# Kernel tuning notes

Measured on AMD Instinct MI355X. Metric: run time of the kernel, lower is better.

Reference implementation:

```python
import jax, jax.numpy as jnp
import numpy as np

N = 8192        # n_nodes
F = 256         # n_features
RES_H = 512     # n_res_hidden
REP_H = 256     # n_rep_hidden
EMB = 128       # embed_dim
E = 262144      # n_edges
GAMMA = 0.1


def setup_inputs() -> dict:
    key = jax.random.key(0)
    ks = jax.random.split(key, 20)
    w = lambda k, shape, s=0.05: (jax.random.normal(k, shape, jnp.float32) * s)
    return {
        "x": jax.random.normal(ks[0], (N, F), jnp.float32),
        "edge_index": jax.random.randint(ks[1], (2, E), 0, N),
        # res_model: Linear(N,RES_H)+ReLU, Linear(RES_H,F)+ReLU
        "res_W1": w(ks[2], (N, RES_H)), "res_b1": jnp.zeros((RES_H,), jnp.float32),
        "res_W2": w(ks[3], (RES_H, F)), "res_b2": jnp.zeros((F,), jnp.float32),
        "fc_W1": w(ks[4], (F, REP_H)), "fc_b1": jnp.zeros((REP_H,), jnp.float32),
        "fc_W2": w(ks[5], (REP_H, REP_H)), "fc_b2": jnp.zeros((REP_H,), jnp.float32),
        # rep_gcn: GCNConv(F,REP_H,norm=False), GCNConv(REP_H,REP_H), GCNConv(REP_H,EMB)
        "g_W0": w(ks[6], (F, REP_H)), "g_b0": jnp.zeros((REP_H,), jnp.float32),
        "g_W1": w(ks[7], (REP_H, REP_H)), "g_b1": jnp.zeros((REP_H,), jnp.float32),
        "g_W2": w(ks[8], (REP_H, EMB)), "g_b2": jnp.zeros((EMB,), jnp.float32),
        # dec_fc: Linear(EMB,REP_H)+ReLU, Linear(REP_H,F)+ReLU
        "dec_W1": w(ks[9], (EMB, REP_H)), "dec_b1": jnp.zeros((REP_H,), jnp.float32),
        "dec_W2": w(ks[10], (REP_H, F)), "dec_b2": jnp.zeros((F,), jnp.float32),
    }


def _gcn(h, src, dst, W, b, normalize):
    """PyG GCNConv: transform then aggregate src->dst; sym-norm with self loops if normalize."""
    h = h @ W
    if normalize:
        ones = jnp.ones(src.shape[0], h.dtype)
        deg = jax.ops.segment_sum(ones, dst, num_segments=N) + 1.0  # +1 self loop
        dinv = jax.lax.rsqrt(deg)
        coef = dinv[src] * dinv[dst]
        agg = jax.ops.segment_sum(h[src] * coef[:, None], dst, num_segments=N)
        agg = agg + h * (dinv * dinv)[:, None]  # self-loop message
    else:
        agg = jax.ops.segment_sum(h[src], dst, num_segments=N)
    return agg + b


def _fwd(x, edge_index, res_W1, res_b1, res_W2, res_b2, fc_W1, fc_b1, fc_W2, fc_b2,
         g_W0, g_b0, g_W1, g_b1, g_W2, g_b2, dec_W1, dec_b1, dec_W2, dec_b2):
    relu = jax.nn.relu
    src, dst = edge_index[0], edge_index[1]
    # dense adjacency (to_dense_adj accumulates edge weights = 1)
    A = jnp.zeros((N, N), x.dtype).at[src, dst].add(1.0)
    # residual model over adjacency rows
    R = relu(relu(A @ res_W1 + res_b1) @ res_W2 + res_b2)  # [N, F]
    # GCN layer 0 (normalize=False)
    H = relu(_gcn(x, src, dst, g_W0, g_b0, False))
    # layer 1
    R_l = relu(R @ fc_W1 + fc_b1)
    H = relu(_gcn(H * jnp.exp(-GAMMA * R_l), src, dst, g_W1, g_b1, True))
    # layer 2
    R_l = relu(R_l @ fc_W2 + fc_b2)
    H = relu(_gcn(H * jnp.exp(-GAMMA * R_l), src, dst, g_W2, g_b2, True))  # [N, EMB]
    X_hat = relu(relu(H @ dec_W1 + dec_b1) @ dec_W2 + dec_b2)  # [N, F]
    A_hat = H @ H.T  # [N, N]
    return X_hat, A_hat, R


def reference(x, edge_index, res_W1, res_b1, res_W2, res_b2, fc_W1, fc_b1, fc_W2, fc_b2,
              g_W0, g_b0, g_W1, g_b1, g_W2, g_b2, dec_W1, dec_b1, dec_W2, dec_b2):
    return _fwd(x, edge_index, res_W1, res_b1, res_W2, res_b2, fc_W1, fc_b1, fc_W2, fc_b2,
                g_W0, g_b0, g_W1, g_b1, g_W2, g_b2, dec_W1, dec_b1, dec_W2, dec_b2)
```

## Files before the change

kernel.cpp:

```cpp
#include <hip/hip_runtime.h>
#include <cstddef>
#include <cstdint>
#include <math.h>

#define NN   8192
#define FF   256
#define RESH 512
#define REPH 256
#define EMBD 128
#define EE   262144
#define GAMMA_ 0.1f

typedef __attribute__((ext_vector_type(8))) short bf16x8;
typedef __attribute__((ext_vector_type(4))) float f32x4;
typedef __attribute__((ext_vector_type(4))) short s16x4;

__device__ inline void f2hilo(float x, short& h, short& l) {
  unsigned u = __float_as_uint(x);
  unsigned r = u + 0x7FFFu + ((u >> 16) & 1u);
  h = (short)(r >> 16);
  float hf = __uint_as_float(r & 0xFFFF0000u);
  float lf = x - hf;
  unsigned u2 = __float_as_uint(lf);
  unsigned r2 = u2 + 0x7FFFu + ((u2 >> 16) & 1u);
  l = (short)(r2 >> 16);
}


__global__ void count_kernel(const int* __restrict__ ei, int* __restrict__ cnt_src,
                             int* __restrict__ cnt_dst) {
  int e = blockIdx.x * blockDim.x + threadIdx.x;
  if (e < EE) {
    atomicAdd(&cnt_src[ei[e]], 1);
    atomicAdd(&cnt_dst[ei[EE + e]], 1);
  }
}

__global__ void scan_kernel(const int* __restrict__ cnt_src, const int* __restrict__ cnt_dst,
                            int* __restrict__ off_src, int* __restrict__ off_dst) {
  const int* cnt = blockIdx.x ? cnt_dst : cnt_src;
  int* off = blockIdx.x ? off_dst : off_src;
  __shared__ int sm[1024];
  int carry = 0;
  for (int ch = 0; ch < NN / 1024; ++ch) {
    int idx = ch * 1024 + threadIdx.x;
    int v = cnt[idx];
    int x = v;
    sm[threadIdx.x] = x;
    __syncthreads();
    for (int ofs = 1; ofs < 1024; ofs <<= 1) {
      int y = (threadIdx.x >= ofs) ? sm[threadIdx.x - ofs] : 0;
      __syncthreads();
      x += y;
      sm[threadIdx.x] = x;
      __syncthreads();
    }
    off[idx] = x - v + carry;
    carry += sm[1023];
    __syncthreads();
  }
  if (threadIdx.x == 0) off[NN] = carry;
}

__global__ void fill_kernel(const int* __restrict__ ei, const int* __restrict__ off_src,
                            const int* __restrict__ off_dst, int* __restrict__ cur_src,
                            int* __restrict__ cur_dst, int* __restrict__ adj_src,
                            int* __restrict__ adj_dst) {
  int e = blockIdx.x * blockDim.x + threadIdx.x;
  if (e < EE) {
    int s = ei[e], d = ei[EE + e];
    int ps = atomicAdd(&cur_src[s], 1);
    adj_src[off_src[s] + ps] = d;
    int pd = atomicAdd(&cur_dst[d], 1);
    adj_dst[off_dst[d] + pd] = s;
  }
}

__global__ void dinv_kernel(const int* __restrict__ cnt_dst, float* __restrict__ dinv) {
  int n = blockIdx.x * blockDim.x + threadIdx.x;
  if (n < NN) dinv[n] = rsqrtf((float)cnt_dst[n] + 1.0f);
}

__global__ __launch_bounds__(256) void s1_kernel(const float* __restrict__ W1,
    const float* __restrict__ b1, const int* __restrict__ off_src,
    const int* __restrict__ adj_src, short* __restrict__ S1h, short* __restrict__ S1l) {
  int i = blockIdx.x, t = threadIdx.x;
  int beg = off_src[i], end = off_src[i + 1];
  float a0 = 0.f, a1 = 0.f;
#pragma unroll 4
  for (int k = beg; k < end; ++k) {
    int d = adj_src[k];
    const float* row = W1 + (size_t)d * RESH;
    a0 += row[t];
    a1 += row[t + 256];
  }
  float v0 = fmaxf(a0 + b1[t], 0.f);
  float v1 = fmaxf(a1 + b1[t + 256], 0.f);
  short hh, ll;
  f2hilo(v0, hh, ll);
  S1h[(size_t)i * RESH + t] = hh;
  S1l[(size_t)i * RESH + t] = ll;
  f2hilo(v1, hh, ll);
  S1h[(size_t)i * RESH + t + 256] = hh;
  S1l[(size_t)i * RESH + t + 256] = ll;
}

__global__ __launch_bounds__(256) void agg0_fused(const float* __restrict__ h,
    const float* __restrict__ b, const float* __restrict__ mod,
    const int* __restrict__ off_dst, const int* __restrict__ adj_dst,
    short* __restrict__ oh, short* __restrict__ ol) {
  int d = blockIdx.x, t = threadIdx.x;
  int beg = off_dst[d], end = off_dst[d + 1];
  float acc = 0.f;
#pragma unroll 4
  for (int k = beg; k < end; ++k) {
    int s = adj_dst[k];
    acc += h[(size_t)s * REPH + t];
  }
  size_t o = (size_t)d * REPH + t;
  float v = fmaxf(acc + b[t], 0.f) * expf(-GAMMA_ * mod[o]);
  short hh, ll;
  f2hilo(v, hh, ll);
  oh[o] = hh;
  ol[o] = ll;
}

__global__ void aggn_fused(const float* __restrict__ h, const float* __restrict__ b,
    const float* __restrict__ dinv, const float* __restrict__ mod,
    const int* __restrict__ off_dst, const int* __restrict__ adj_dst,
    short* __restrict__ oh, short* __restrict__ ol, int C) {
  int d = blockIdx.x, t = threadIdx.x;
  int beg = off_dst[d], end = off_dst[d + 1];
  float acc = 0.f;
#pragma unroll 4
  for (int k = beg; k < end; ++k) {
    int s = adj_dst[k];
    acc += h[(size_t)s * C + t] * dinv[s];
  }
  float dd = dinv[d];
  size_t o = (size_t)d * C + t;
  float v = fmaxf(acc * dd + h[o] * dd * dd + b[t], 0.f);
  if (mod) v *= expf(-GAMMA_ * mod[o]);
  short hh, ll;
  f2hilo(v, hh, ll);
  oh[o] = hh;
  ol[o] = ll;
}

struct WDesc { const float* src; short* h; short* l; int K; int N; };
struct WTab { WDesc d[8]; };

__global__ void prep_w(WTab tab) {
  WDesc d = tab.d[blockIdx.y];
  int total = d.K * d.N;
  for (int i = blockIdx.x * 256 + threadIdx.x; i < total; i += 128 * 256) {
    int n = i / d.K, k = i - n * d.K;
    float x = d.src[(size_t)k * d.N + n];
    short hh, ll;
    f2hilo(x, hh, ll);
    d.h[i] = hh;
    d.l[i] = ll;
  }
}

__global__ void conv_split(const float* __restrict__ in, short* __restrict__ oh,
                           short* __restrict__ ol) {
  int i = (blockIdx.x * 256 + threadIdx.x) * 4;
  f32x4 v = *(const f32x4*)(in + i);
  s16x4 vh, vl;
#pragma unroll
  for (int j = 0; j < 4; ++j) {
    short hh, ll;
    f2hilo(v[j], hh, ll);
    vh[j] = hh;
    vl[j] = ll;
  }
  *(s16x4*)(oh + i) = vh;
  *(s16x4*)(ol + i) = vl;
}

template<int CB>
__global__ __launch_bounds__(256) void gemmS(const short* __restrict__ Ah,
    const short* __restrict__ Al, const short* __restrict__ Wh,
    const short* __restrict__ Wl, const float* __restrict__ bias, int doRelu,
    float* __restrict__ outF, short* __restrict__ outH, short* __restrict__ outL,
    int K, int Nc) {
  const int w = threadIdx.x >> 6, l = threadIdx.x & 63;
  const int lr = l & 15, lk = l >> 4;
  const int m0 = blockIdx.y * 64 + w * 16;
  const int n0 = blockIdx.x * (CB * 16);
  f32x4 acc[CB] = {};
  const int nks = K >> 5;
  for (int ks = 0; ks < nks; ++ks) {
    const int k0 = (ks << 5) + (lk << 3);
    size_t aoff = (size_t)(m0 + lr) * K + k0;
    bf16x8 ah = *(const bf16x8*)(Ah + aoff);
    bf16x8 al = *(const bf16x8*)(Al + aoff);
#pragma unroll
    for (int cb = 0; cb < CB; ++cb) {
      size_t boff = (size_t)(n0 + (cb << 4) + lr) * K + k0;
      bf16x8 bh = *(const bf16x8*)(Wh + boff);
      bf16x8 bl = *(const bf16x8*)(Wl + boff);
      acc[cb] = __builtin_amdgcn_mfma_f32_16x16x32_bf16(ah, bh, acc[cb], 0, 0, 0);
      acc[cb] = __builtin_amdgcn_mfma_f32_16x16x32_bf16(al, bh, acc[cb], 0, 0, 0);
      acc[cb] = __builtin_amdgcn_mfma_f32_16x16x32_bf16(ah, bl, acc[cb], 0, 0, 0);
    }
  }
#pragma unroll
  for (int cb = 0; cb < CB; ++cb) {
    int col = n0 + (cb << 4) + lr;
    float bv = bias ? bias[col] : 0.f;
#pragma unroll
    for (int r = 0; r < 4; ++r) {
      int row = m0 + (lk << 2) + r;
      float v = acc[cb][r] + bv;
      if (doRelu) v = fmaxf(v, 0.f);
      size_t off = (size_t)row * Nc + col;
      if (outF) outF[off] = v;
      if (outH) {
        short hh, ll;
        f2hilo(v, hh, ll);
        outH[off] = hh;
        outL[off] = ll;
      }
    }
  }
}

__global__ __launch_bounds__(256) void ahat_sym(const short* __restrict__ Hh,
    const short* __restrict__ Hl, float* __restrict__ C) {
  __shared__ float sm[128][129];
  int z = blockIdx.x;
  int b = (int)((sqrtf(8.f * (float)z + 1.f) - 1.f) * 0.5f);
  while ((b + 1) * (b + 2) / 2 <= z) ++b;
  while (b * (b + 1) / 2 > z) --b;
  int a = z - b * (b + 1) / 2;
  const int bi = a * 128, bj = b * 128;
  const bool mirror = (a != b);
  const int w = threadIdx.x >> 6, l = threadIdx.x & 63;
  const int lr = l & 15, lk = l >> 4;
  const int ri = w * 32;
  f32x4 acc[2][8] = {};
#pragma unroll
  for (int ks = 0; ks < 4; ++ks) {
    const int k0 = (ks << 5) + (lk << 3);
    bf16x8 ah[2], al[2];
#pragma unroll
    for (int rb = 0; rb < 2; ++rb) {
      size_t off = (size_t)(bi + ri + (rb << 4) + lr) * EMBD + k0;
      ah[rb] = *(const bf16x8*)(Hh + off);
      al[rb] = *(const bf16x8*)(Hl + off);
    }
#pragma unroll
    for (int cb = 0; cb < 8; ++cb) {
      size_t off = (size_t)(bj + (cb << 4) + lr) * EMBD + k0;
      bf16x8 bh = *(const bf16x8*)(Hh + off);
      bf16x8 bl = *(const bf16x8*)(Hl + off);
#pragma unroll
      for (int rb = 0; rb < 2; ++rb) {
        acc[rb][cb] = __builtin_amdgcn_mfma_f32_16x16x32_bf16(ah[rb], bh, acc[rb][cb], 0, 0, 0);
        acc[rb][cb] = __builtin_amdgcn_mfma_f32_16x16x32_bf16(al[rb], bh, acc[rb][cb], 0, 0, 0);
        acc[rb][cb] = __builtin_amdgcn_mfma_f32_16x16x32_bf16(ah[rb], bl, acc[rb][cb], 0, 0, 0);
      }
    }
  }
#pragma unroll
  for (int rb = 0; rb < 2; ++rb)
#pragma unroll
    for (int cb = 0; cb < 8; ++cb) {
      int r0 = ri + (rb << 4) + (lk << 2);
      int c0 = (cb << 4) + lr;
#pragma unroll
      for (int r = 0; r < 4; ++r) {
        float v = acc[rb][cb][r];
        C[(size_t)(bi + r0 + r) * NN + bj + c0] = v;
        if (mirror) sm[r0 + r][c0] = v;
      }
    }
  if (mirror) {
    __syncthreads();
    for (int idx = threadIdx.x; idx < 128 * 128; idx += 256) {
      int jr = idx >> 7, c = idx & 127;
      C[(size_t)(bj + jr) * NN + bi + c] = sm[c][jr];
    }
  }
}


extern "C" void kernel_launch(void* const* d_in, const int* in_sizes, int n_in,
                              void* d_out, int out_size, void* d_ws, size_t ws_size,
                              hipStream_t stream) {
  const float* x      = (const float*)d_in[0];
  const int*   ei     = (const int*)d_in[1];
  const float* res_W1 = (const float*)d_in[2];
  const float* res_b1 = (const float*)d_in[3];
  const float* res_W2 = (const float*)d_in[4];
  const float* res_b2 = (const float*)d_in[5];
  const float* fc_W1  = (const float*)d_in[6];
  const float* fc_b1  = (const float*)d_in[7];
  const float* fc_W2  = (const float*)d_in[8];
  const float* fc_b2  = (const float*)d_in[9];
  const float* g_W0   = (const float*)d_in[10];
  const float* g_b0   = (const float*)d_in[11];
  const float* g_W1   = (const float*)d_in[12];
  const float* g_b1   = (const float*)d_in[13];
  const float* g_W2   = (const float*)d_in[14];
  const float* g_b2   = (const float*)d_in[15];
  const float* dec_W1 = (const float*)d_in[16];
  const float* dec_b1 = (const float*)d_in[17];
  const float* dec_W2 = (const float*)d_in[18];
  const float* dec_b2 = (const float*)d_in[19];

  float* out   = (float*)d_out;
  float* X_hat = out;
  float* A_hat = out + (size_t)NN * FF;
  float* R     = A_hat + (size_t)NN * NN;

  char* ws = (char*)d_ws;
  size_t o = 0;
  auto alloc = [&](size_t bytes) -> void* {
    void* p = ws + o;
    o += (bytes + 1023) & ~(size_t)1023;
    return p;
  };
  int* cnt_src = (int*)alloc(NN * 4);
  int* cnt_dst = (int*)alloc(NN * 4);
  int* cur_src = (int*)alloc(NN * 4);
  int* cur_dst = (int*)alloc(NN * 4);
  int* off_src = (int*)alloc((NN + 1) * 4);
  int* off_dst = (int*)alloc((NN + 1) * 4);
  int* adj_src = (int*)alloc((size_t)EE * 4);
  int* adj_dst = (int*)alloc((size_t)EE * 4);
  float* dinv  = (float*)alloc(NN * 4);
  short* Wt_h  = (short*)alloc(524288 * 2);
  short* Wt_l  = (short*)alloc(524288 * 2);
  const size_t SLAB = (size_t)8 * 1024 * 1024;
  char* slabA = (char*)alloc(SLAB);
  char* slabB = (char*)alloc(SLAB);
  char* slabC = (char*)alloc(SLAB);
  char* slabD = (char*)alloc(SLAB);
  short* S1h = (short*)slabA;
  short* Xh  = (short*)slabA;            short* Xl  = (short*)(slabA + SLAB / 2);
  short* M1h = (short*)slabA;            short* M1l = (short*)(slabA + SLAB / 2);
  short* M2h = (short*)slabA;            short* M2l = (short*)(slabA + SLAB / 2);
  short* D1h = (short*)slabA;            short* D1l = (short*)(slabA + SLAB / 2);
  short* S1l = (short*)slabB;
  float* B3f = (float*)slabB;
  float* B4f = (float*)slabB;
  float* G2f = (float*)slabB;
  short* Rh  = (short*)slabC;            short* Rl  = (short*)(slabC + SLAB / 2);
  float* B1f = (float*)slabC;
  float* G1f = (float*)slabC;
  short* B3h = (short*)slabD;            short* B3l = (short*)(slabD + SLAB / 2);
  short* Hh  = (short*)slabD;            short* Hl  = (short*)(slabD + (size_t)2 * 1024 * 1024);

  const int o_resW2 = 0;
  const int o_fcW1  = 131072;
  const int o_fcW2  = 196608;
  const int o_gW0   = 262144;
  const int o_gW1   = 327680;
  const int o_gW2   = 393216;
  const int o_decW1 = 425984;
  const int o_decW2 = 458752;

  hipMemsetAsync(cnt_src, 0, (size_t)NN * 4 * 4, stream);

  count_kernel<<<EE / 256, 256, 0, stream>>>(ei, cnt_src, cnt_dst);
  scan_kernel<<<2, 1024, 0, stream>>>(cnt_src, cnt_dst, off_src, off_dst);
  fill_kernel<<<EE / 256, 256, 0, stream>>>(ei, off_src, off_dst, cur_src, cur_dst,
                                            adj_src, adj_dst);
  dinv_kernel<<<NN / 256, 256, 0, stream>>>(cnt_dst, dinv);

  WTab tab;
  tab.d[0] = {res_W2, Wt_h + o_resW2, Wt_l + o_resW2, RESH, FF};
  tab.d[1] = {fc_W1,  Wt_h + o_fcW1,  Wt_l + o_fcW1,  FF,   REPH};
  tab.d[2] = {fc_W2,  Wt_h + o_fcW2,  Wt_l + o_fcW2,  REPH, REPH};
  tab.d[3] = {g_W0,   Wt_h + o_gW0,   Wt_l + o_gW0,   FF,   REPH};
  tab.d[4] = {g_W1,   Wt_h + o_gW1,   Wt_l + o_gW1,   REPH, REPH};
  tab.d[5] = {g_W2,   Wt_h + o_gW2,   Wt_l + o_gW2,   REPH, EMBD};
  tab.d[6] = {dec_W1, Wt_h + o_decW1, Wt_l + o_decW1, EMBD, REPH};
  tab.d[7] = {dec_W2, Wt_h + o_decW2, Wt_l + o_decW2, REPH, FF};
  prep_w<<<dim3(128, 8), 256, 0, stream>>>(tab);

  s1_kernel<<<NN, 256, 0, stream>>>(res_W1, res_b1, off_src, adj_src, S1h, S1l);
  gemmS<8><<<dim3(2, 128), 256, 0, stream>>>(S1h, S1l, Wt_h + o_resW2, Wt_l + o_resW2,
      res_b2, 1, R, Rh, Rl, RESH, FF);
  gemmS<8><<<dim3(2, 128), 256, 0, stream>>>(Rh, Rl, Wt_h + o_fcW1, Wt_l + o_fcW1,
      fc_b1, 1, B3f, B3h, B3l, FF, REPH);
  conv_split<<<(NN * FF) / 1024, 256, 0, stream>>>(x, Xh, Xl);
  gemmS<8><<<dim3(2, 128), 256, 0, stream>>>(Xh, Xl, Wt_h + o_gW0, Wt_l + o_gW0,
      nullptr, 0, B1f, nullptr, nullptr, FF, REPH);
  agg0_fused<<<NN, REPH, 0, stream>>>(B1f, g_b0, B3f, off_dst, adj_dst, M1h, M1l);
  gemmS<8><<<dim3(2, 128), 256, 0, stream>>>(M1h, M1l, Wt_h + o_gW1, Wt_l + o_gW1,
      nullptr, 0, G1f, nullptr, nullptr, REPH, REPH);
  gemmS<8><<<dim3(2, 128), 256, 0, stream>>>(B3h, B3l, Wt_h + o_fcW2, Wt_l + o_fcW2,
      fc_b2, 1, B4f, nullptr, nullptr, REPH, REPH);
  aggn_fused<<<NN, REPH, 0, stream>>>(G1f, g_b1, dinv, B4f, off_dst, adj_dst,
                                      M2h, M2l, REPH);
  gemmS<4><<<dim3(2, 128), 256, 0, stream>>>(M2h, M2l, Wt_h + o_gW2, Wt_l + o_gW2,
      nullptr, 0, G2f, nullptr, nullptr, REPH, EMBD);
  aggn_fused<<<NN, EMBD, 0, stream>>>(G2f, g_b2, dinv, nullptr, off_dst, adj_dst,
                                      Hh, Hl, EMBD);
  gemmS<8><<<dim3(2, 128), 256, 0, stream>>>(Hh, Hl, Wt_h + o_decW1, Wt_l + o_decW1,
      dec_b1, 1, nullptr, D1h, D1l, EMBD, REPH);
  gemmS<8><<<dim3(2, 128), 256, 0, stream>>>(D1h, D1l, Wt_h + o_decW2, Wt_l + o_decW2,
      dec_b2, 1, X_hat, nullptr, nullptr, REPH, FF);
  ahat_sym<<<2080, 256, 0, stream>>>(Hh, Hl, A_hat);
}
```

Before: 800.2 us.

## Vectorize gather-aggregation kernels and split edge lists across wavefronts

The four gather kernels (adjacency-row sum and three GCN aggregations) are rewritten so each lane loads float4 or float2 chunks of a neighbour row. The edge list is split across the block's wavefronts, each unrolled by four, and partial sums are reduced through shared memory. The aim is more memory-level parallelism and fewer load instructions per edge. dinv is now computed inside the scan kernel, which removes one launch. The cost is a shared-memory reduction plus a sync, and only one wavefront does the epilogue.

```diff
diff --git a/kernel.cpp b/kernel.cpp
--- a/kernel.cpp
+++ b/kernel.cpp
@@ -13,7 +13,9 @@
 
 typedef __attribute__((ext_vector_type(8))) short bf16x8;
 typedef __attribute__((ext_vector_type(4))) float f32x4;
+typedef __attribute__((ext_vector_type(2))) float f32x2;
 typedef __attribute__((ext_vector_type(4))) short s16x4;
+typedef __attribute__((ext_vector_type(2))) short s16x2;
 
 __device__ inline void f2hilo(float x, short& h, short& l) {
   unsigned u = __float_as_uint(x);
@@ -37,7 +39,8 @@
 }
 
 __global__ void scan_kernel(const int* __restrict__ cnt_src, const int* __restrict__ cnt_dst,
-                            int* __restrict__ off_src, int* __restrict__ off_dst) {
+                            int* __restrict__ off_src, int* __restrict__ off_dst,
+                            float* __restrict__ dinv) {
   const int* cnt = blockIdx.x ? cnt_dst : cnt_src;
   int* off = blockIdx.x ? off_dst : off_src;
   __shared__ int sm[1024];
@@ -45,6 +48,7 @@
   for (int ch = 0; ch < NN / 1024; ++ch) {
     int idx = ch * 1024 + threadIdx.x;
     int v = cnt[idx];
+    if (blockIdx.x) dinv[idx] = rsqrtf((float)v + 1.0f);
     int x = v;
     sm[threadIdx.x] = x;
     __syncthreads();
@@ -76,75 +80,181 @@
   }
 }
 
-__global__ void dinv_kernel(const int* __restrict__ cnt_dst, float* __restrict__ dinv) {
-  int n = blockIdx.x * blockDim.x + threadIdx.x;
-  if (n < NN) dinv[n] = rsqrtf((float)cnt_dst[n] + 1.0f);
-}
-
-__global__ __launch_bounds__(256) void s1_kernel(const float* __restrict__ W1,
+__global__ __launch_bounds__(256) void s1_v2(const float* __restrict__ W1,
     const float* __restrict__ b1, const int* __restrict__ off_src,
     const int* __restrict__ adj_src, short* __restrict__ S1h, short* __restrict__ S1l) {
-  int i = blockIdx.x, t = threadIdx.x;
-  int beg = off_src[i], end = off_src[i + 1];
-  float a0 = 0.f, a1 = 0.f;
-#pragma unroll 4
-  for (int k = beg; k < end; ++k) {
-    int d = adj_src[k];
-    const float* row = W1 + (size_t)d * RESH;
-    a0 += row[t];
-    a1 += row[t + 256];
-  }
-  float v0 = fmaxf(a0 + b1[t], 0.f);
-  float v1 = fmaxf(a1 + b1[t + 256], 0.f);
-  short hh, ll;
-  f2hilo(v0, hh, ll);
-  S1h[(size_t)i * RESH + t] = hh;
-  S1l[(size_t)i * RESH + t] = ll;
-  f2hilo(v1, hh, ll);
-  S1h[(size_t)i * RESH + t + 256] = hh;
-  S1l[(size_t)i * RESH + t + 256] = ll;
-}
-
-__global__ __launch_bounds__(256) void agg0_fused(const float* __restrict__ h,
+  __shared__ f32x4 p2[2][64];
+  const int i = blockIdx.x, w = threadIdx.x >> 6, lane = threadIdx.x & 63;
+  const int half = w & 1, par = w >> 1;
+  const int col = half * 256 + lane * 4;
+  const float* base = W1 + col;
+  const int beg = off_src[i], end = off_src[i + 1];
+  f32x4 acc = {};
+  int k = beg + par;
+  for (; k + 6 < end; k += 8) {
+    int s0 = adj_src[k], s1 = adj_src[k + 2], s2 = adj_src[k + 4], s3 = adj_src[k + 6];
+    f32x4 h0 = *(const f32x4*)(base + (size_t)s0 * RESH);
+    f32x4 h1 = *(const f32x4*)(base + (size_t)s1 * RESH);
+    f32x4 h2 = *(const f32x4*)(base + (size_t)s2 * RESH);
+    f32x4 h3 = *(const f32x4*)(base + (size_t)s3 * RESH);
+    acc += h0 + h1 + h2 + h3;
+  }
+  for (; k < end; k += 2) {
+    int s = adj_src[k];
+    acc += *(const f32x4*)(base + (size_t)s * RESH);
+  }
+  if (par == 1) p2[half][lane] = acc;
+  __syncthreads();
+  if (par == 0) {
+    acc += p2[half][lane];
+    f32x4 bb = *(const f32x4*)(b1 + col);
+    s16x4 vh, vl;
+#pragma unroll
+    for (int j = 0; j < 4; ++j) {
+      float v = fmaxf(acc[j] + bb[j], 0.f);
+      short hh, ll;
+      f2hilo(v, hh, ll);
+      vh[j] = hh; vl[j] = ll;
+    }
+    size_t o = (size_t)i * RESH + col;
+    *(s16x4*)(S1h + o) = vh;
+    *(s16x4*)(S1l + o) = vl;
+  }
+}
+
+__global__ __launch_bounds__(256) void agg0_v2(const float* __restrict__ h,
     const float* __restrict__ b, const float* __restrict__ mod,
     const int* __restrict__ off_dst, const int* __restrict__ adj_dst,
     short* __restrict__ oh, short* __restrict__ ol) {
-  int d = blockIdx.x, t = threadIdx.x;
-  int beg = off_dst[d], end = off_dst[d + 1];
-  float acc = 0.f;
-#pragma unroll 4
-  for (int k = beg; k < end; ++k) {
+  __shared__ f32x4 part[3][64];
+  const int d = blockIdx.x, w = threadIdx.x >> 6, lane = threadIdx.x & 63;
+  const float* base = h + lane * 4;
+  const int beg = off_dst[d], end = off_dst[d + 1];
+  f32x4 acc = {};
+  int k = beg + w;
+  for (; k + 12 < end; k += 16) {
+    int s0 = adj_dst[k], s1 = adj_dst[k + 4], s2 = adj_dst[k + 8], s3 = adj_dst[k + 12];
+    f32x4 h0 = *(const f32x4*)(base + (size_t)s0 * REPH);
+    f32x4 h1 = *(const f32x4*)(base + (size_t)s1 * REPH);
+    f32x4 h2 = *(const f32x4*)(base + (size_t)s2 * REPH);
+    f32x4 h3 = *(const f32x4*)(base + (size_t)s3 * REPH);
+    acc += h0 + h1 + h2 + h3;
+  }
+  for (; k < end; k += 4) {
     int s = adj_dst[k];
-    acc += h[(size_t)s * REPH + t];
-  }
-  size_t o = (size_t)d * REPH + t;
-  float v = fmaxf(acc + b[t], 0.f) * expf(-GAMMA_ * mod[o]);
-  short hh, ll;
-  f2hilo(v, hh, ll);
-  oh[o] = hh;
-  ol[o] = ll;
-}
-
-__global__ void aggn_fused(const float* __restrict__ h, const float* __restrict__ b,
-    const float* __restrict__ dinv, const float* __restrict__ mod,
+    acc += *(const f32x4*)(base + (size_t)s * REPH);
+  }
+  if (w) part[w - 1][lane] = acc;
+  __syncthreads();
+  if (w == 0) {
+    acc += part[0][lane] + part[1][lane] + part[2][lane];
+    size_t o = (size_t)d * REPH + lane * 4;
+    f32x4 bb = *(const f32x4*)(b + lane * 4);
+    f32x4 mm = *(const f32x4*)(mod + o);
+    s16x4 vh, vl;
+#pragma unroll
+    for (int j = 0; j < 4; ++j) {
+      float v = fmaxf(acc[j] + bb[j], 0.f) * expf(-GAMMA_ * mm[j]);
+      short hh, ll;
+      f2hilo(v, hh, ll);
+      vh[j] = hh; vl[j] = ll;
+    }
+    *(s16x4*)(oh + o) = vh;
+    *(s16x4*)(ol + o) = vl;
+  }
+}
+
+__global__ __launch_bounds__(256) void aggn256_v2(const float* __restrict__ h,
+    const float* __restrict__ b, const float* __restrict__ dinv,
+    const float* __restrict__ mod, const int* __restrict__ off_dst,
+    const int* __restrict__ adj_dst, short* __restrict__ oh, short* __restrict__ ol) {
+  __shared__ f32x4 part[3][64];
+  const int d = blockIdx.x, w = threadIdx.x >> 6, lane = threadIdx.x & 63;
+  const float* base = h + lane * 4;
+  const int beg = off_dst[d], end = off_dst[d + 1];
+  f32x4 acc = {};
+  int k = beg + w;
+  for (; k + 12 < end; k += 16) {
+    int s0 = adj_dst[k], s1 = adj_dst[k + 4], s2 = adj_dst[k + 8], s3 = adj_dst[k + 12];
+    float d0 = dinv[s0], d1 = dinv[s1], d2 = dinv[s2], d3 = dinv[s3];
+    f32x4 h0 = *(const f32x4*)(base + (size_t)s0 * REPH);
+    f32x4 h1 = *(const f32x4*)(base + (size_t)s1 * REPH);
+    f32x4 h2 = *(const f32x4*)(base + (size_t)s2 * REPH);
+    f32x4 h3 = *(const f32x4*)(base + (size_t)s3 * REPH);
+    acc += h0 * d0 + h1 * d1 + h2 * d2 + h3 * d3;
+  }
+  for (; k < end; k += 4) {
+    int s = adj_dst[k];
+    acc += *(const f32x4*)(base + (size_t)s * REPH) * dinv[s];
+  }
+  if (w) part[w - 1][lane] = acc;
+  __syncthreads();
+  if (w == 0) {
+    acc += part[0][lane] + part[1][lane] + part[2][lane];
+    const float dd = dinv[d];
+    size_t o = (size_t)d * REPH + lane * 4;
+    f32x4 bb = *(const f32x4*)(b + lane * 4);
+    f32x4 self = *(const f32x4*)(h + o);
+    s16x4 vh, vl;
+    if (mod) {
+      f32x4 mm = *(const f32x4*)(mod + o);
+#pragma unroll
+      for (int j = 0; j < 4; ++j) {
+        float v = fmaxf(acc[j] * dd + self[j] * dd * dd + bb[j], 0.f) * expf(-GAMMA_ * mm[j]);
+        short hh, ll; f2hilo(v, hh, ll); vh[j] = hh; vl[j] = ll;
+      }
+    } else {
+#pragma unroll
+      for (int j = 0; j < 4; ++j) {
+        float v = fmaxf(acc[j] * dd + self[j] * dd * dd + bb[j], 0.f);
+        short hh, ll; f2hilo(v, hh, ll); vh[j] = hh; vl[j] = ll;
+      }
+    }
+    *(s16x4*)(oh + o) = vh;
+    *(s16x4*)(ol + o) = vl;
+  }
+}
+
+__global__ __launch_bounds__(256) void aggn128_v2(const float* __restrict__ h,
+    const float* __restrict__ b, const float* __restrict__ dinv,
     const int* __restrict__ off_dst, const int* __restrict__ adj_dst,
-    short* __restrict__ oh, short* __restrict__ ol, int C) {
-  int d = blockIdx.x, t = threadIdx.x;
-  int beg = off_dst[d], end = off_dst[d + 1];
-  float acc = 0.f;
-#pragma unroll 4
-  for (int k = beg; k < end; ++k) {
+    short* __restrict__ oh, short* __restrict__ ol) {
+  __shared__ f32x2 part[3][64];
+  const int d = blockIdx.x, w = threadIdx.x >> 6, lane = threadIdx.x & 63;
+  const float* base = h + lane * 2;
+  const int beg = off_dst[d], end = off_dst[d + 1];
+  f32x2 acc = {};
+  int k = beg + w;
+  for (; k + 12 < end; k += 16) {
+    int s0 = adj_dst[k], s1 = adj_dst[k + 4], s2 = adj_dst[k + 8], s3 = adj_dst[k + 12];
+    float d0 = dinv[s0], d1 = dinv[s1], d2 = dinv[s2], d3 = dinv[s3];
+    f32x2 h0 = *(const f32x2*)(base + (size_t)s0 * EMBD);
+    f32x2 h1 = *(const f32x2*)(base + (size_t)s1 * EMBD);
+    f32x2 h2 = *(const f32x2*)(base + (size_t)s2 * EMBD);
+    f32x2 h3 = *(const f32x2*)(base + (size_t)s3 * EMBD);
+    acc += h0 * d0 + h1 * d1 + h2 * d2 + h3 * d3;
+  }
+  for (; k < end; k += 4) {
     int s = adj_dst[k];
-    acc += h[(size_t)s * C + t] * dinv[s];
-  }
-  float dd = dinv[d];
-  size_t o = (size_t)d * C + t;
-  float v = fmaxf(acc * dd + h[o] * dd * dd + b[t], 0.f);
-  if (mod) v *= expf(-GAMMA_ * mod[o]);
-  short hh, ll;
-  f2hilo(v, hh, ll);
-  oh[o] = hh;
-  ol[o] = ll;
+    acc += *(const f32x2*)(base + (size_t)s * EMBD) * dinv[s];
+  }
+  if (w) part[w - 1][lane] = acc;
+  __syncthreads();
+  if (w == 0) {
+    acc += part[0][lane] + part[1][lane] + part[2][lane];
+    const float dd = dinv[d];
+    size_t o = (size_t)d * EMBD + lane * 2;
+    f32x2 bb = *(const f32x2*)(b + lane * 2);
+    f32x2 self = *(const f32x2*)(h + o);
+    s16x2 vh, vl;
+#pragma unroll
+    for (int j = 0; j < 2; ++j) {
+      float v = fmaxf(acc[j] * dd + self[j] * dd * dd + bb[j], 0.f);
+      short hh, ll; f2hilo(v, hh, ll); vh[j] = hh; vl[j] = ll;
+    }
+    *(s16x2*)(oh + o) = vh;
+    *(s16x2*)(ol + o) = vl;
+  }
 }
 
 struct WDesc { const float* src; short* h; short* l; int K; int N; };
@@ -366,10 +476,9 @@
   hipMemsetAsync(cnt_src, 0, (size_t)NN * 4 * 4, stream);
 
   count_kernel<<<EE / 256, 256, 0, stream>>>(ei, cnt_src, cnt_dst);
-  scan_kernel<<<2, 1024, 0, stream>>>(cnt_src, cnt_dst, off_src, off_dst);
+  scan_kernel<<<2, 1024, 0, stream>>>(cnt_src, cnt_dst, off_src, off_dst, dinv);
   fill_kernel<<<EE / 256, 256, 0, stream>>>(ei, off_src, off_dst, cur_src, cur_dst,
                                             adj_src, adj_dst);
-  dinv_kernel<<<NN / 256, 256, 0, stream>>>(cnt_dst, dinv);
 
   WTab tab;
   tab.d[0] = {res_W2, Wt_h + o_resW2, Wt_l + o_resW2, RESH, FF};
@@ -382,7 +491,7 @@
   tab.d[7] = {dec_W2, Wt_h + o_decW2, Wt_l + o_decW2, REPH, FF};
   prep_w<<<dim3(128, 8), 256, 0, stream>>>(tab);
 
-  s1_kernel<<<NN, 256, 0, stream>>>(res_W1, res_b1, off_src, adj_src, S1h, S1l);
+  s1_v2<<<NN, 256, 0, stream>>>(res_W1, res_b1, off_src, adj_src, S1h, S1l);
   gemmS<8><<<dim3(2, 128), 256, 0, stream>>>(S1h, S1l, Wt_h + o_resW2, Wt_l + o_resW2,
       res_b2, 1, R, Rh, Rl, RESH, FF);
   gemmS<8><<<dim3(2, 128), 256, 0, stream>>>(Rh, Rl, Wt_h + o_fcW1, Wt_l + o_fcW1,
@@ -390,17 +499,15 @@
   conv_split<<<(NN * FF) / 1024, 256, 0, stream>>>(x, Xh, Xl);
   gemmS<8><<<dim3(2, 128), 256, 0, stream>>>(Xh, Xl, Wt_h + o_gW0, Wt_l + o_gW0,
       nullptr, 0, B1f, nullptr, nullptr, FF, REPH);
-  agg0_fused<<<NN, REPH, 0, stream>>>(B1f, g_b0, B3f, off_dst, adj_dst, M1h, M1l);
+  agg0_v2<<<NN, 256, 0, stream>>>(B1f, g_b0, B3f, off_dst, adj_dst, M1h, M1l);
   gemmS<8><<<dim3(2, 128), 256, 0, stream>>>(M1h, M1l, Wt_h + o_gW1, Wt_l + o_gW1,
       nullptr, 0, G1f, nullptr, nullptr, REPH, REPH);
   gemmS<8><<<dim3(2, 128), 256, 0, stream>>>(B3h, B3l, Wt_h + o_fcW2, Wt_l + o_fcW2,
       fc_b2, 1, B4f, nullptr, nullptr, REPH, REPH);
-  aggn_fused<<<NN, REPH, 0, stream>>>(G1f, g_b1, dinv, B4f, off_dst, adj_dst,
-                                      M2h, M2l, REPH);
+  aggn256_v2<<<NN, 256, 0, stream>>>(G1f, g_b1, dinv, B4f, off_dst, adj_dst, M2h, M2l);
   gemmS<4><<<dim3(2, 128), 256, 0, stream>>>(M2h, M2l, Wt_h + o_gW2, Wt_l + o_gW2,
       nullptr, 0, G2f, nullptr, nullptr, REPH, EMBD);
-  aggn_fused<<<NN, EMBD, 0, stream>>>(G2f, g_b2, dinv, nullptr, off_dst, adj_dst,
-                                      Hh, Hl, EMBD);
+  aggn128_v2<<<NN, 256, 0, stream>>>(G2f, g_b2, dinv, off_dst, adj_dst, Hh, Hl);
   gemmS<8><<<dim3(2, 128), 256, 0, stream>>>(Hh, Hl, Wt_h + o_decW1, Wt_l + o_decW1,
       dec_b1, 1, nullptr, D1h, D1l, EMBD, REPH);
   gemmS<8><<<dim3(2, 128), 256, 0, stream>>>(D1h, D1l, Wt_h + o_decW2, Wt_l + o_decW2,
```

New measurement: 787.5 us. No clear change (-1.6%).
